# Performance work log

Measured on AMD Instinct MI355X. Metric: run time of the kernel, lower is better.

The kernel has to match this reference:

```python
import jax, jax.numpy as jnp
import numpy as np

B, T, HW = 16, 64, 7
D = 768          # input_dim == base_dim
N = 12           # num_heads
C = D // N       # head_dim = 64
EPS = 1e-5


def layernorm(x, g, b):
    m = jnp.mean(x, axis=-1, keepdims=True)
    v = jnp.mean((x - m) ** 2, axis=-1, keepdims=True)
    return (x - m) * jax.lax.rsqrt(v + EPS) * g + b


def setup_inputs() -> dict:
    key = jax.random.key(0)
    ks = jax.random.split(key, 12)
    s = lambda k, shape: (jax.random.normal(k, shape, jnp.float32) * 0.02)
    return {
        "x": jax.random.normal(ks[0], (B, T, HW, HW, D), jnp.float32),
        "W_qkv": s(ks[1], (D, 3 * D)),                  # qkv_bias=False
        "Wpq": s(ks[2], (C, C, HW, HW)), "bpq": jnp.zeros((C,), jnp.float32),
        "Wpk": s(ks[3], (C, C, HW, HW)), "bpk": jnp.zeros((C,), jnp.float32),
        "Wpv": s(ks[4], (C, C, HW, HW)), "bpv": jnp.zeros((C,), jnp.float32),
        "g_q": jnp.ones((C,), jnp.float32), "be_q": jnp.zeros((C,), jnp.float32),
        "g_k": jnp.ones((C,), jnp.float32), "be_k": jnp.zeros((C,), jnp.float32),
        "g_v": jnp.ones((C,), jnp.float32), "be_v": jnp.zeros((C,), jnp.float32),
        "rel_pos_t": s(ks[5], (2 * T - 1, C)),          # (127, 64): matches dt, no interp
        "W_proj": s(ks[6], (D, D)), "b_proj": jnp.zeros((D,), jnp.float32),
    }


def reference(x, W_qkv, Wpq, bpq, Wpk, bpk, Wpv, bpv,
              g_q, be_q, g_k, be_k, g_v, be_v, rel_pos_t, W_proj, b_proj):
    b, t = x.shape[0], x.shape[1]
    # qkv projection -> (B,T,H,W,3,N,C)
    qkv = (x @ W_qkv).reshape(b, t, HW, HW, 3, N, C)
    q3, k3, v3 = qkv[..., 0, :, :], qkv[..., 1, :, :], qkv[..., 2, :, :]  # (B,T,H,W,N,C)
    # Conv3d kernel (1,7,7) on full 7x7 spatial == contraction over (h,w,c_in)
    q = jnp.einsum('bthwnc,dchw->bntd', q3, Wpq) + bpq   # (B,N,T,C)
    k = jnp.einsum('bthwnc,dchw->bntd', k3, Wpk) + bpk
    v = jnp.einsum('bthwnc,dchw->bntd', v3, Wpv) + bpv
    q = layernorm(q, g_q, be_q)
    k = layernorm(k, g_k, be_k)
    v = layernorm(v, g_v, be_v)
    scale = C ** -0.5
    attn = jnp.einsum('bntc,bnsc->bnts', q * scale, k)   # (B,N,T,T)
    # relative temporal position bias: gather table rows by distance, matmul with q
    dist = jnp.arange(t)[:, None] - jnp.arange(t)[None, :] + (t - 1)  # (T,T) in [0,2T-2]
    Rt = rel_pos_t[dist]                                  # (T,T,C)
    rel = jnp.einsum('bntc,tsc->bnts', q, Rt)
    attn = jax.nn.softmax(attn + rel, axis=-1)
    out = jnp.einsum('bnts,bnsc->bntc', attn, v) + q      # residual add of q
    out = out.transpose(0, 2, 1, 3).reshape(b, t, N * C)  # (B,T,D)
    return out @ W_proj + b_proj
```

## Files before the change

### kernel.cpp

```cpp
#include <hip/hip_runtime.h>


typedef __attribute__((ext_vector_type(8))) short bf16x8;
typedef __attribute__((ext_vector_type(4))) float f32x4;

#define AS1U(p) ((const __attribute__((address_space(1))) unsigned int*)(p))
#define AS3U(p) ((__attribute__((address_space(3))) unsigned int*)(p))

__device__ __forceinline__ unsigned short cvt_bf16(float x) {
  union { float f; unsigned int u; } v; v.f = x;
  unsigned int r = v.u + 0x7fffu + ((v.u >> 16) & 1u);
  return (unsigned short)(r >> 16);
}
__device__ __forceinline__ float bf2f(unsigned short h) {
  union { unsigned int u; float f; } v; v.u = ((unsigned int)h) << 16;
  return v.f;
}

__device__ __forceinline__ void wg_barrier() {
  asm volatile("" ::: "memory");
  __builtin_amdgcn_s_barrier();
  asm volatile("" ::: "memory");
}

__global__ __launch_bounds__(256) void cvt_x_k(const float* __restrict__ src,
                                               unsigned short* __restrict__ dst, int n8) {
  int i = blockIdx.x * 256 + threadIdx.x;
  if (i >= n8) return;
  const float4* s = (const float4*)src + (size_t)i * 2;
  float4 a = s[0], b = s[1];
  ushort4 r0 = { cvt_bf16(a.x), cvt_bf16(a.y), cvt_bf16(a.z), cvt_bf16(a.w) };
  ushort4 r1 = { cvt_bf16(b.x), cvt_bf16(b.y), cvt_bf16(b.z), cvt_bf16(b.w) };
  ushort4* d = (ushort4*)dst + (size_t)i * 2;
  d[0] = r0; d[1] = r1;
}

__global__ __launch_bounds__(256) void transpose_cvt_k(const float* __restrict__ src,
                                                       unsigned short* __restrict__ dst) {
  __shared__ float tl[32][33];
  int k0 = blockIdx.x * 32, n0 = blockIdx.y * 32;
  int tx = threadIdx.x & 31, ty = threadIdx.x >> 5;
#pragma unroll
  for (int r = 0; r < 32; r += 8)
    tl[ty + r][tx] = src[(size_t)(k0 + ty + r) * 2304 + n0 + tx];
  __syncthreads();
#pragma unroll
  for (int r = 0; r < 32; r += 8)
    dst[(size_t)(n0 + ty + r) * 768 + k0 + tx] = cvt_bf16(tl[tx][ty + r]);
}

__global__ __launch_bounds__(256) void prep_cvt_k(
    const float* __restrict__ Wpq, const float* __restrict__ Wpk,
    const float* __restrict__ Wpv, const float* __restrict__ relp,
    unsigned short* __restrict__ WpTT, unsigned short* __restrict__ relb) {
  int bid = blockIdx.x;
  if (bid < 2400) {
    int p = bid / 800;
    const float* src = (p == 0) ? Wpq : (p == 1) ? Wpk : Wpv;
    unsigned short* dst = WpTT + (size_t)p * 204800;
    int o = (bid - p * 800) * 256 + threadIdx.x;
    if (o >= 204800) return;
    int c = o & 63, d = (o >> 6) & 63, hw = o >> 12;
    dst[o] = (hw < 49) ? cvt_bf16(src[d * 3136 + c * 49 + hw]) : (unsigned short)0;
  } else {
    int i = (bid - 2400) * 256 + threadIdx.x;
    relb[i] = (i < 8128) ? cvt_bf16(relp[i]) : (unsigned short)0;
  }
}

__global__ __launch_bounds__(512, 2) void gemm_qkv_8ph(
    const unsigned short* __restrict__ A, const unsigned short* __restrict__ Bt,
    unsigned short* __restrict__ Cb) {
  __shared__ unsigned short As[2][16384];
  __shared__ unsigned short Bs[2][16384];

  const int orig = blockIdx.x;
  const int xcd = orig & 7;
  const int lid = orig >> 3;
  const int wgid = (xcd < 4 ? xcd * 221 : 884 + (xcd - 4) * 220) + lid;
  const int mb = wgid / 9, nb = wgid % 9;
  const int m0 = mb * 256, n0 = nb * 256;
  const int K = 768;

  const int tid = threadIdx.x;
  const int wave = tid >> 6, lane = tid & 63;
  const int quad = lane >> 4, l16 = lane & 15;
  const int wr = wave >> 2, wc = wave & 3;
  const int x7 = l16 & 7;

  const int srow = tid >> 3;
  const int cs = (tid & 7) ^ (srow & 7);
  const unsigned short* Ag[4];
  const unsigned short* Bg[4];
#pragma unroll
  for (int l = 0; l < 4; ++l) {
    Ag[l] = A + (size_t)(m0 + l * 64 + srow) * K + cs * 8;
    Bg[l] = Bt + (size_t)(n0 + l * 64 + srow) * K + cs * 8;
  }
  const int ldst = wave * 512;

#define STAGE(buf, kt) do {                                                        \
    const int ko_ = (kt) * 64;                                                     \
    _Pragma("unroll")                                                              \
    for (int l_ = 0; l_ < 4; ++l_) {                                               \
      __builtin_amdgcn_global_load_lds(AS1U(Ag[l_] + ko_),                         \
          AS3U(&As[buf][l_ * 4096 + ldst]), 16, 0, 0);                             \
      __builtin_amdgcn_global_load_lds(AS1U(Bg[l_] + ko_),                         \
          AS3U(&Bs[buf][l_ * 4096 + ldst]), 16, 0, 0);                             \
    }                                                                              \
  } while (0)

#define LDA(buf, mi) do {                                                          \
    _Pragma("unroll")                                                              \
    for (int fi_ = 0; fi_ < 4; ++fi_) {                                            \
      const int row_ = wr * 128 + (mi) * 64 + fi_ * 16 + l16;                      \
      _Pragma("unroll")                                                            \
      for (int ks_ = 0; ks_ < 2; ++ks_)                                            \
        af[fi_][ks_] = *(const bf16x8*)&As[buf][row_ * 64 +                        \
            (((ks_ * 4 + quad) ^ x7) * 8)];                                        \
    }                                                                              \
  } while (0)

#define LDB(buf, nj) do {                                                          \
    _Pragma("unroll")                                                              \
    for (int fj_ = 0; fj_ < 2; ++fj_) {                                            \
      const int row_ = wc * 64 + (nj) * 32 + fj_ * 16 + l16;                       \
      _Pragma("unroll")                                                            \
      for (int ks_ = 0; ks_ < 2; ++ks_)                                            \
        bfv[nj][fj_][ks_] = *(const bf16x8*)&Bs[buf][row_ * 64 +                   \
            (((ks_ * 4 + quad) ^ x7) * 8)];                                        \
    }                                                                              \
  } while (0)

#define MFMAQ(mi, nj) do {                                                         \
    _Pragma("unroll")                                                              \
    for (int ks_ = 0; ks_ < 2; ++ks_)                                              \
      _Pragma("unroll")                                                            \
      for (int fi_ = 0; fi_ < 4; ++fi_)                                            \
        _Pragma("unroll")                                                          \
        for (int fj_ = 0; fj_ < 2; ++fj_)                                          \
          acc[(mi) * 4 + fi_][(nj) * 2 + fj_] =                                    \
              __builtin_amdgcn_mfma_f32_16x16x32_bf16(af[fi_][ks_],                \
                  bfv[nj][fj_][ks_], acc[(mi) * 4 + fi_][(nj) * 2 + fj_], 0, 0, 0);\
  } while (0)

#define ITER(cur, DO_STAGE, kt2, VMI) do {                                         \
    asm volatile("s_waitcnt vmcnt(" #VMI ")" ::: "memory");                        \
    wg_barrier();                                                                  \
                                                                           \
    LDA(cur, 0); LDB(cur, 0);                                                      \
    wg_barrier();                                                                  \
    __builtin_amdgcn_s_setprio(1); MFMAQ(0, 0); __builtin_amdgcn_s_setprio(0);     \
    wg_barrier();                                                                  \
                                                                           \
    LDB(cur, 1);                                                                   \
    wg_barrier();                                                                  \
    __builtin_amdgcn_s_setprio(1); MFMAQ(0, 1); __builtin_amdgcn_s_setprio(0);     \
    wg_barrier();                                                                  \
                                                                           \
    LDA(cur, 1);                                                                   \
    wg_barrier();                                                                  \
    __builtin_amdgcn_s_setprio(1); MFMAQ(1, 0); __builtin_amdgcn_s_setprio(0);     \
    wg_barrier();                                                                  \
             \
    if (DO_STAGE) STAGE(cur, kt2);                                                 \
    __builtin_amdgcn_s_setprio(1); MFMAQ(1, 1); __builtin_amdgcn_s_setprio(0);     \
    wg_barrier();                                                                  \
  } while (0)

  f32x4 acc[8][4];
#pragma unroll
  for (int i = 0; i < 8; ++i)
#pragma unroll
    for (int j = 0; j < 4; ++j) acc[i][j] = (f32x4){0.f, 0.f, 0.f, 0.f};
  bf16x8 af[4][2];
  bf16x8 bfv[2][2][2];

  STAGE(0, 0);
  STAGE(1, 1);

  for (int kt = 0; kt < 10; kt += 2) {
    ITER(0, true, kt + 2, 8);
    ITER(1, true, kt + 3, 8);
  }
  ITER(0, false, 0, 8);
  ITER(1, false, 0, 0);

#undef ITER
#undef MFMAQ
#undef LDB
#undef LDA
#undef STAGE

#pragma unroll
  for (int i = 0; i < 8; ++i)
#pragma unroll
    for (int j = 0; j < 4; ++j)
#pragma unroll
      for (int r = 0; r < 4; ++r) {
        int row = m0 + wr * 128 + i * 16 + quad * 4 + r;
        int col = n0 + wc * 64 + j * 16 + l16;
        Cb[(size_t)row * 2304 + col] = cvt_bf16(acc[i][j][r]);
      }
}

__global__ __launch_bounds__(256) void pool_ln_mfma_k(
    const unsigned short* __restrict__ qkvb, const unsigned short* __restrict__ WpTT,
    const float* __restrict__ bq, const float* __restrict__ bk, const float* __restrict__ bv,
    const float* __restrict__ gq, const float* __restrict__ gk, const float* __restrict__ gv,
    const float* __restrict__ beq, const float* __restrict__ bek, const float* __restrict__ bev,
    unsigned short* __restrict__ oq, unsigned short* __restrict__ ok_,
    unsigned short* __restrict__ ov) {
  __shared__ float smem_f[16384];
  __shared__ float mu_s[64], rs_s[64];
  unsigned short* AB = (unsigned short*)smem_f;
  float* Ln = smem_f;

  const int n = blockIdx.x, p = blockIdx.y, b = blockIdx.z;
  const int tid = threadIdx.x;
  const int wave = tid >> 6, lane = tid & 63;
  const int quad = lane >> 4, l16 = lane & 15;
  const int wm = (wave >> 1) * 32, wn = (wave & 1) * 32;

  const int lr = lane >> 4, lg = lane & 15;
  const size_t abase = ((size_t)b * 3136) * 2304 + (size_t)p * 768 + (size_t)n * 64;
  const unsigned short* WpB = WpTT + (size_t)p * 204800;

  const unsigned short* pA[4];
  const unsigned short* pB[4];
#pragma unroll
  for (int q = 0; q < 4; ++q) {
    int r = wave * 16 + q * 4 + lr;
    int g = lg ^ (r & 15);
    pA[q] = qkvb + abase + (size_t)r * 112896 + (size_t)(g >> 3) * 2304 + (g & 7) * 8;
    pB[q] = WpB + (size_t)(g >> 3) * 4096 + r * 64 + (g & 7) * 8;
  }

#define PSTAGE(buf, it) do {                                                       \
    const size_t offA_ = (size_t)(it) * 4608;                                      \
    const size_t offB_ = (size_t)(it) * 8192;                                      \
    unsigned short* Ad_ = AB + (buf) * 8192;                                       \
    unsigned short* Bd_ = AB + 16384 + (buf) * 8192;                               \
    _Pragma("unroll")                                                              \
    for (int q_ = 0; q_ < 4; ++q_) {                                               \
      __builtin_amdgcn_global_load_lds(AS1U(pA[q_] + offA_),                       \
          AS3U(&Ad_[(wave * 16 + q_ * 4) * 128]), 16, 0, 0);                       \
      __builtin_amdgcn_global_load_lds(AS1U(pB[q_] + offB_),                       \
          AS3U(&Bd_[(wave * 16 + q_ * 4) * 128]), 16, 0, 0);                       \
    }                                                                              \
  } while (0)

#define PCOMPUTE(buf) do {                                                         \
    const unsigned short* Ad_ = AB + (buf) * 8192;                                 \
    const unsigned short* Bd_ = AB + 16384 + (buf) * 8192;                         \
    bf16x8 af_[2][4], bf_[2][4];                                                   \
    _Pragma("unroll")                                                              \
    for (int f_ = 0; f_ < 2; ++f_) {                                               \
      int ra_ = wm + f_ * 16 + l16;                                                \
      int rb_ = wn + f_ * 16 + l16;                                                \
      _Pragma("unroll")                                                            \
      for (int ki_ = 0; ki_ < 4; ++ki_) {                                          \
        af_[f_][ki_] = *(const bf16x8*)&Ad_[ra_ * 128 +                            \
            (((ki_ * 4 + quad) ^ (ra_ & 15)) * 8)];                                \
        bf_[f_][ki_] = *(const bf16x8*)&Bd_[rb_ * 128 +                            \
            (((ki_ * 4 + quad) ^ (rb_ & 15)) * 8)];                                \
      }                                                                            \
    }                                                                              \
    _Pragma("unroll")                                                              \
    for (int ki_ = 0; ki_ < 4; ++ki_)                                              \
      _Pragma("unroll")                                                            \
      for (int i_ = 0; i_ < 2; ++i_)                                               \
        _Pragma("unroll")                                                          \
        for (int j_ = 0; j_ < 2; ++j_)                                             \
          acc[i_][j_] = __builtin_amdgcn_mfma_f32_16x16x32_bf16(                   \
              af_[i_][ki_], bf_[j_][ki_], acc[i_][j_], 0, 0, 0);                   \
  } while (0)

  f32x4 acc[2][2];
#pragma unroll
  for (int i = 0; i < 2; ++i)
#pragma unroll
    for (int j = 0; j < 2; ++j) acc[i][j] = (f32x4){0.f, 0.f, 0.f, 0.f};

  PSTAGE(0, 0);
  for (int it2 = 0; it2 < 24; it2 += 2) {
    PSTAGE(1, it2 + 1);
    asm volatile("s_waitcnt vmcnt(8)" ::: "memory");
    wg_barrier();
    PCOMPUTE(0);
    wg_barrier();
    PSTAGE(0, it2 + 2);
    asm volatile("s_waitcnt vmcnt(8)" ::: "memory");
    wg_barrier();
    PCOMPUTE(1);
    wg_barrier();
  }
  asm volatile("s_waitcnt vmcnt(0)" ::: "memory");
  wg_barrier();
  PCOMPUTE(0);
  __syncthreads();

#undef PCOMPUTE
#undef PSTAGE

  const float* bias = (p == 0) ? bq : (p == 1) ? bk : bv;
  const float* g    = (p == 0) ? gq : (p == 1) ? gk : gv;
  const float* be   = (p == 0) ? beq : (p == 1) ? bek : bev;
  unsigned short* outp = (p == 0) ? oq : (p == 1) ? ok_ : ov;

#pragma unroll
  for (int i = 0; i < 2; ++i)
#pragma unroll
    for (int j = 0; j < 2; ++j)
#pragma unroll
      for (int r = 0; r < 4; ++r) {
        int t = wm + i * 16 + quad * 4 + r;
        int d = wn + j * 16 + l16;
        Ln[t * 65 + d] = acc[i][j][r] + bias[d];
      }
  __syncthreads();
  if (tid < 64) {
    float s = 0.f;
#pragma unroll 8
    for (int c = 0; c < 64; ++c) s += Ln[tid * 65 + c];
    float m = s * (1.f / 64.f);
    float v2 = 0.f;
#pragma unroll 8
    for (int c = 0; c < 64; ++c) { float dl = Ln[tid * 65 + c] - m; v2 += dl * dl; }
    mu_s[tid] = m;
    rs_s[tid] = rsqrtf(v2 * (1.f / 64.f) + 1e-5f);
  }
  __syncthreads();
  {
    int t = tid >> 2, d0 = (tid & 3) * 16;
    float m = mu_s[t], rv = rs_s[t];
    unsigned short ob[16];
#pragma unroll
    for (int j = 0; j < 16; ++j)
      ob[j] = cvt_bf16((Ln[t * 65 + d0 + j] - m) * rv * g[d0 + j] + be[d0 + j]);
    unsigned short* dst = outp + ((size_t)(b * 12 + n) * 64 + t) * 64 + d0;
    *(uint4*)dst = *(uint4*)ob;
    *(uint4*)(dst + 8) = *(uint4*)(ob + 8);
  }
}

__global__ __launch_bounds__(256) void attn_mfma_k(
    const unsigned short* __restrict__ qp, const unsigned short* __restrict__ kp,
    const unsigned short* __restrict__ vp, const unsigned short* __restrict__ relb,
    float* __restrict__ aout) {
  __shared__ unsigned short qs[64 * 64];
  __shared__ unsigned short ks[64 * 64];
  __shared__ unsigned short vt[64 * 64];
  __shared__ unsigned short rs[128 * 64];
  __shared__ float Gs[64 * 128];
  __shared__ unsigned short Ps[64 * 64];

  const int n = blockIdx.x, b = blockIdx.y;
  const int tid = threadIdx.x;
  const size_t base = ((size_t)b * 12 + n) * 4096;

  for (int i = tid; i < 512; i += 256) {
    ((uint4*)qs)[i] = ((const uint4*)(qp + base))[i];
    ((uint4*)ks)[i] = ((const uint4*)(kp + base))[i];
  }
  for (int i = tid; i < 1024; i += 256)
    ((uint4*)rs)[i] = ((const uint4*)relb)[i];
  {
    int s = tid >> 2, c0 = (tid & 3) * 16;
    unsigned short tmp[16];
    *(uint4*)tmp = *(const uint4*)(vp + base + s * 64 + c0);
    *(uint4*)(tmp + 8) = *(const uint4*)(vp + base + s * 64 + c0 + 8);
#pragma unroll
    for (int i = 0; i < 16; ++i) vt[(c0 + i) * 64 + s] = tmp[i];
  }
  __syncthreads();

  const int wave = tid >> 6, lane = tid & 63;
  const int quad = lane >> 4, l16 = lane & 15;
  const int tm = wave * 16;

  bf16x8 aq[2];
  aq[0] = *(const bf16x8*)&qs[(tm + l16) * 64 + quad * 8];
  aq[1] = *(const bf16x8*)&qs[(tm + l16) * 64 + quad * 8 + 32];

  f32x4 accqk[4], accg[8];
#pragma unroll
  for (int j = 0; j < 4; ++j) accqk[j] = (f32x4){0.f, 0.f, 0.f, 0.f};
#pragma unroll
  for (int j = 0; j < 8; ++j) accg[j] = (f32x4){0.f, 0.f, 0.f, 0.f};

#pragma unroll
  for (int ki = 0; ki < 2; ++ki) {
#pragma unroll
    for (int j = 0; j < 4; ++j) {
      bf16x8 bk = *(const bf16x8*)&ks[(j * 16 + l16) * 64 + quad * 8 + ki * 32];
      accqk[j] = __builtin_amdgcn_mfma_f32_16x16x32_bf16(aq[ki], bk, accqk[j], 0, 0, 0);
    }
#pragma unroll
    for (int j = 0; j < 8; ++j) {
      bf16x8 br = *(const bf16x8*)&rs[(j * 16 + l16) * 64 + quad * 8 + ki * 32];
      accg[j] = __builtin_amdgcn_mfma_f32_16x16x32_bf16(aq[ki], br, accg[j], 0, 0, 0);
    }
  }
#pragma unroll
  for (int j = 0; j < 8; ++j)
#pragma unroll
    for (int r = 0; r < 4; ++r)
      Gs[(tm + quad * 4 + r) * 128 + j * 16 + l16] = accg[j][r];
  __syncthreads();

#pragma unroll
  for (int r = 0; r < 4; ++r) {
    int t = tm + quad * 4 + r;
    float sv[4];
#pragma unroll
    for (int j = 0; j < 4; ++j) {
      int s = j * 16 + l16;
      sv[j] = 0.125f * accqk[j][r] + Gs[t * 128 + (t + 63 - s)];
    }
    float m = fmaxf(fmaxf(sv[0], sv[1]), fmaxf(sv[2], sv[3]));
    m = fmaxf(m, __shfl_xor(m, 1));
    m = fmaxf(m, __shfl_xor(m, 2));
    m = fmaxf(m, __shfl_xor(m, 4));
    m = fmaxf(m, __shfl_xor(m, 8));
    float e[4], sum = 0.f;
#pragma unroll
    for (int j = 0; j < 4; ++j) { e[j] = __expf(sv[j] - m); sum += e[j]; }
    sum += __shfl_xor(sum, 1);
    sum += __shfl_xor(sum, 2);
    sum += __shfl_xor(sum, 4);
    sum += __shfl_xor(sum, 8);
    float inv = 1.f / sum;
#pragma unroll
    for (int j = 0; j < 4; ++j)
      Ps[t * 64 + j * 16 + l16] = cvt_bf16(e[j] * inv);
  }
  __syncthreads();

  bf16x8 ap[2];
  ap[0] = *(const bf16x8*)&Ps[(tm + l16) * 64 + quad * 8];
  ap[1] = *(const bf16x8*)&Ps[(tm + l16) * 64 + quad * 8 + 32];
  f32x4 acco[4];
#pragma unroll
  for (int j = 0; j < 4; ++j) acco[j] = (f32x4){0.f, 0.f, 0.f, 0.f};
#pragma unroll
  for (int ki = 0; ki < 2; ++ki)
#pragma unroll
    for (int j = 0; j < 4; ++j) {
      bf16x8 bv = *(const bf16x8*)&vt[(j * 16 + l16) * 64 + quad * 8 + ki * 32];
      acco[j] = __builtin_amdgcn_mfma_f32_16x16x32_bf16(ap[ki], bv, acco[j], 0, 0, 0);
    }
#pragma unroll
  for (int j = 0; j < 4; ++j)
#pragma unroll
    for (int r = 0; r < 4; ++r) {
      int t = tm + quad * 4 + r;
      int c = j * 16 + l16;
      float o = acco[j][r] + bf2f(qs[t * 64 + c]);
      aout[((size_t)b * 64 + t) * 768 + n * 64 + c] = o;
    }
}

__global__ __launch_bounds__(256) void gemm_f32_k(
    const float* __restrict__ A, const float* __restrict__ Bm,
    const float* __restrict__ bias, float* __restrict__ Cm,
    int M, int Nn, int K) {
  __shared__ float As[16][68];
  __shared__ float Bs[16][64];
  const int tid = threadIdx.x;
  const int ty = tid >> 4, tx = tid & 15;
  const int m0 = blockIdx.y * 64, n0 = blockIdx.x * 64;

  const int la_m = tid >> 2;
  const int la_k = (tid & 3) << 2;
  const int lb_k = tid >> 4;
  const int lb_n = (tid & 15) << 2;

  const float* Ap = A + (size_t)(m0 + la_m) * K + la_k;
  const float* Bp = Bm + (size_t)lb_k * Nn + n0 + lb_n;

  float acc[4][4];
#pragma unroll
  for (int i = 0; i < 4; ++i)
#pragma unroll
    for (int j = 0; j < 4; ++j) acc[i][j] = 0.f;

  for (int k0 = 0; k0 < K; k0 += 16) {
    float4 av = *(const float4*)(Ap + k0);
    float4 bv = *(const float4*)(Bp + (size_t)k0 * Nn);
    As[la_k + 0][la_m] = av.x;
    As[la_k + 1][la_m] = av.y;
    As[la_k + 2][la_m] = av.z;
    As[la_k + 3][la_m] = av.w;
    *(float4*)&Bs[lb_k][lb_n] = bv;
    __syncthreads();
#pragma unroll
    for (int kk = 0; kk < 16; ++kk) {
      float af[4], bf[4];
      *(float4*)af = *(const float4*)&As[kk][ty << 2];
      *(float4*)bf = *(const float4*)&Bs[kk][tx << 2];
#pragma unroll
      for (int i = 0; i < 4; ++i)
#pragma unroll
        for (int j = 0; j < 4; ++j) acc[i][j] += af[i] * bf[j];
    }
    __syncthreads();
  }

  float bb[4] = {0.f, 0.f, 0.f, 0.f};
  if (bias) {
#pragma unroll
    for (int j = 0; j < 4; ++j) bb[j] = bias[n0 + (tx << 2) + j];
  }
#pragma unroll
  for (int i = 0; i < 4; ++i) {
    float4 o;
    o.x = acc[i][0] + bb[0];
    o.y = acc[i][1] + bb[1];
    o.z = acc[i][2] + bb[2];
    o.w = acc[i][3] + bb[3];
    *(float4*)(Cm + (size_t)(m0 + (ty << 2) + i) * Nn + n0 + (tx << 2)) = o;
  }
}

extern "C" void kernel_launch(void* const* d_in, const int* in_sizes, int n_in,
                              void* d_out, int out_size, void* d_ws, size_t ws_size,
                              hipStream_t stream) {
  const float* x     = (const float*)d_in[0];
  const float* Wqkv  = (const float*)d_in[1];
  const float* Wpq   = (const float*)d_in[2];
  const float* bpq   = (const float*)d_in[3];
  const float* Wpk   = (const float*)d_in[4];
  const float* bpk   = (const float*)d_in[5];
  const float* Wpv   = (const float*)d_in[6];
  const float* bpv   = (const float*)d_in[7];
  const float* gq    = (const float*)d_in[8];
  const float* beq   = (const float*)d_in[9];
  const float* gk    = (const float*)d_in[10];
  const float* bek   = (const float*)d_in[11];
  const float* gv    = (const float*)d_in[12];
  const float* bev   = (const float*)d_in[13];
  const float* relp  = (const float*)d_in[14];
  const float* Wproj = (const float*)d_in[15];
  const float* bproj = (const float*)d_in[16];
  float* out = (float*)d_out;

  unsigned short* u = (unsigned short*)d_ws;
  unsigned short* xbf   = u;
  unsigned short* qkvbf = u + 38535168ull;
  unsigned short* WqkvT = u + 154140672ull;
  unsigned short* WpTT  = u + 155910144ull;
  unsigned short* relb  = u + 156524544ull;
  unsigned short* qpb   = u + 156532736ull;
  unsigned short* kpb   = u + 157319168ull;
  unsigned short* vpb   = u + 158105600ull;
  float* aout = (float*)(u + 158892032ull);

  cvt_x_k<<<18816, 256, 0, stream>>>(x, xbf, 4816896);
  transpose_cvt_k<<<dim3(24, 72), 256, 0, stream>>>(Wqkv, WqkvT);
  prep_cvt_k<<<2432, 256, 0, stream>>>(Wpq, Wpk, Wpv, relp, WpTT, relb);

  gemm_qkv_8ph<<<1764, 512, 0, stream>>>(xbf, WqkvT, qkvbf);

  pool_ln_mfma_k<<<dim3(12, 3, 16), 256, 0, stream>>>(
      qkvbf, WpTT, bpq, bpk, bpv, gq, gk, gv, beq, bek, bev, qpb, kpb, vpb);

  attn_mfma_k<<<dim3(12, 16), 256, 0, stream>>>(qpb, kpb, vpb, relb, aout);

  gemm_f32_k<<<dim3(12, 16), 256, 0, stream>>>(aout, Wproj, bproj, out, 1024, 768, 768);
}
```

Baseline: 617.2 us.

## Shrink QKV GEMM tile to 128x128 with 256 threads and XCD-aware mapping

Replaces the 256x256, 512-thread QKV projection GEMM with a 128x128 tile on 256 threads, launching four times as many workgroups. Tiles are now assigned so each XCD owns a contiguous band of row blocks across all column blocks. Staging is split into separate A and B loads placed at different points in the four-phase MFMA schedule, and fragments are held in separate register arrays for the two halves. The smaller tile cuts LDS and registers per workgroup, allowing more occupancy and better load balance. The cost is lower arithmetic intensity per tile and more global and L2 traffic.

```diff
diff --git a/kernel.cpp b/kernel.cpp
--- a/kernel.cpp
+++ b/kernel.cpp
@@ -68,24 +68,24 @@
   }
 }
 
-__global__ __launch_bounds__(512, 2) void gemm_qkv_8ph(
+__global__ __launch_bounds__(256, 2) void gemm_qkv_128(
     const unsigned short* __restrict__ A, const unsigned short* __restrict__ Bt,
     unsigned short* __restrict__ Cb) {
-  __shared__ unsigned short As[2][16384];
-  __shared__ unsigned short Bs[2][16384];
+  __shared__ unsigned short As[2][8192];
+  __shared__ unsigned short Bs[2][8192];
 
   const int orig = blockIdx.x;
   const int xcd = orig & 7;
-  const int lid = orig >> 3;
-  const int wgid = (xcd < 4 ? xcd * 221 : 884 + (xcd - 4) * 220) + lid;
-  const int mb = wgid / 9, nb = wgid % 9;
-  const int m0 = mb * 256, n0 = nb * 256;
+  const int slot = orig >> 3;
+  const int mb = xcd * 49 + slot / 18;
+  const int nb = slot % 18;
+  const int m0 = mb * 128, n0 = nb * 128;
   const int K = 768;
 
   const int tid = threadIdx.x;
   const int wave = tid >> 6, lane = tid & 63;
   const int quad = lane >> 4, l16 = lane & 15;
-  const int wr = wave >> 2, wc = wave & 3;
+  const int wr = wave >> 1, wc = wave & 1;
   const int x7 = l16 & 7;
 
   const int srow = tid >> 3;
@@ -94,90 +94,99 @@
   const unsigned short* Bg[4];
 #pragma unroll
   for (int l = 0; l < 4; ++l) {
-    Ag[l] = A + (size_t)(m0 + l * 64 + srow) * K + cs * 8;
-    Bg[l] = Bt + (size_t)(n0 + l * 64 + srow) * K + cs * 8;
+    Ag[l] = A + (size_t)(m0 + l * 32 + srow) * K + cs * 8;
+    Bg[l] = Bt + (size_t)(n0 + l * 32 + srow) * K + cs * 8;
   }
   const int ldst = wave * 512;
 
-#define STAGE(buf, kt) do {                                                        \
+#define STAGE_A(buf, kt) do {                                                      \
     const int ko_ = (kt) * 64;                                                     \
     _Pragma("unroll")                                                              \
-    for (int l_ = 0; l_ < 4; ++l_) {                                               \
+    for (int l_ = 0; l_ < 4; ++l_)                                                 \
       __builtin_amdgcn_global_load_lds(AS1U(Ag[l_] + ko_),                         \
-          AS3U(&As[buf][l_ * 4096 + ldst]), 16, 0, 0);                             \
+          AS3U(&As[buf][l_ * 2048 + ldst]), 16, 0, 0);                             \
+  } while (0)
+
+#define STAGE_B(buf, kt) do {                                                      \
+    const int ko_ = (kt) * 64;                                                     \
+    _Pragma("unroll")                                                              \
+    for (int l_ = 0; l_ < 4; ++l_)                                                 \
       __builtin_amdgcn_global_load_lds(AS1U(Bg[l_] + ko_),                         \
-          AS3U(&Bs[buf][l_ * 4096 + ldst]), 16, 0, 0);                             \
-    }                                                                              \
-  } while (0)
-
-#define LDA(buf, mi) do {                                                          \
-    _Pragma("unroll")                                                              \
-    for (int fi_ = 0; fi_ < 4; ++fi_) {                                            \
-      const int row_ = wr * 128 + (mi) * 64 + fi_ * 16 + l16;                      \
+          AS3U(&Bs[buf][l_ * 2048 + ldst]), 16, 0, 0);                             \
+  } while (0)
+
+#define LDA(dst, buf, mi) do {                                                     \
+    _Pragma("unroll")                                                              \
+    for (int fi_ = 0; fi_ < 2; ++fi_) {                                            \
+      const int row_ = wr * 64 + (mi) * 32 + fi_ * 16 + l16;                       \
       _Pragma("unroll")                                                            \
       for (int ks_ = 0; ks_ < 2; ++ks_)                                            \
-        af[fi_][ks_] = *(const bf16x8*)&As[buf][row_ * 64 +                        \
+        dst[fi_][ks_] = *(const bf16x8*)&As[buf][row_ * 64 +                       \
             (((ks_ * 4 + quad) ^ x7) * 8)];                                        \
     }                                                                              \
   } while (0)
 
-#define LDB(buf, nj) do {                                                          \
+#define LDB(dst, buf, nj) do {                                                     \
     _Pragma("unroll")                                                              \
     for (int fj_ = 0; fj_ < 2; ++fj_) {                                            \
       const int row_ = wc * 64 + (nj) * 32 + fj_ * 16 + l16;                       \
       _Pragma("unroll")                                                            \
       for (int ks_ = 0; ks_ < 2; ++ks_)                                            \
-        bfv[nj][fj_][ks_] = *(const bf16x8*)&Bs[buf][row_ * 64 +                   \
+        dst[fj_][ks_] = *(const bf16x8*)&Bs[buf][row_ * 64 +                       \
             (((ks_ * 4 + quad) ^ x7) * 8)];                                        \
     }                                                                              \
   } while (0)
 
-#define MFMAQ(mi, nj) do {                                                         \
+#define MFMAQ(a_, b_, mi, nj) do {                                                 \
     _Pragma("unroll")                                                              \
     for (int ks_ = 0; ks_ < 2; ++ks_)                                              \
       _Pragma("unroll")                                                            \
-      for (int fi_ = 0; fi_ < 4; ++fi_)                                            \
+      for (int fi_ = 0; fi_ < 2; ++fi_)                                            \
         _Pragma("unroll")                                                          \
         for (int fj_ = 0; fj_ < 2; ++fj_)                                          \
-          acc[(mi) * 4 + fi_][(nj) * 2 + fj_] =                                    \
-              __builtin_amdgcn_mfma_f32_16x16x32_bf16(af[fi_][ks_],                \
-                  bfv[nj][fj_][ks_], acc[(mi) * 4 + fi_][(nj) * 2 + fj_], 0, 0, 0);\
+          acc[(mi) * 2 + fi_][(nj) * 2 + fj_] =                                    \
+              __builtin_amdgcn_mfma_f32_16x16x32_bf16(a_[fi_][ks_],                \
+                  b_[fj_][ks_], acc[(mi) * 2 + fi_][(nj) * 2 + fj_], 0, 0, 0);     \
   } while (0)
 
 #define ITER(cur, DO_STAGE, kt2, VMI) do {                                         \
     asm volatile("s_waitcnt vmcnt(" #VMI ")" ::: "memory");                        \
     wg_barrier();                                                                  \
-                                                                           \
-    LDA(cur, 0); LDB(cur, 0);                                                      \
-    wg_barrier();                                                                  \
-    __builtin_amdgcn_s_setprio(1); MFMAQ(0, 0); __builtin_amdgcn_s_setprio(0);     \
-    wg_barrier();                                                                  \
-                                                                           \
-    LDB(cur, 1);                                                                   \
-    wg_barrier();                                                                  \
-    __builtin_amdgcn_s_setprio(1); MFMAQ(0, 1); __builtin_amdgcn_s_setprio(0);     \
-    wg_barrier();                                                                  \
-                                                                           \
-    LDA(cur, 1);                                                                   \
-    wg_barrier();                                                                  \
-    __builtin_amdgcn_s_setprio(1); MFMAQ(1, 0); __builtin_amdgcn_s_setprio(0);     \
-    wg_barrier();                                                                  \
-             \
-    if (DO_STAGE) STAGE(cur, kt2);                                                 \
-    __builtin_amdgcn_s_setprio(1); MFMAQ(1, 1); __builtin_amdgcn_s_setprio(0);     \
-    wg_barrier();                                                                  \
-  } while (0)
-
-  f32x4 acc[8][4];
-#pragma unroll
-  for (int i = 0; i < 8; ++i)
+                                                           \
+    LDA(af0, cur, 0); LDB(bf0, cur, 0);                                            \
+    wg_barrier();                                                                  \
+    __builtin_amdgcn_s_setprio(1); MFMAQ(af0, bf0, 0, 0);                          \
+    __builtin_amdgcn_s_setprio(0);                                                 \
+    wg_barrier();                                                                  \
+                                                           \
+    LDB(bf1, cur, 1);                                                              \
+    wg_barrier();                                                                  \
+    __builtin_amdgcn_s_setprio(1); MFMAQ(af0, bf1, 0, 1);                          \
+    __builtin_amdgcn_s_setprio(0);                                                 \
+    wg_barrier();                                                                  \
+           \
+    LDA(af1, cur, 1);                                                              \
+    if (DO_STAGE) STAGE_B(cur, kt2);                                               \
+    wg_barrier();                                                                  \
+    __builtin_amdgcn_s_setprio(1); MFMAQ(af1, bf0, 1, 0);                          \
+    __builtin_amdgcn_s_setprio(0);                                                 \
+    wg_barrier();                                                                  \
+           \
+    if (DO_STAGE) STAGE_A(cur, kt2);                                               \
+    __builtin_amdgcn_s_setprio(1); MFMAQ(af1, bf1, 1, 1);                          \
+    __builtin_amdgcn_s_setprio(0);                                                 \
+    wg_barrier();                                                                  \
+  } while (0)
+
+  f32x4 acc[4][4];
+#pragma unroll
+  for (int i = 0; i < 4; ++i)
 #pragma unroll
     for (int j = 0; j < 4; ++j) acc[i][j] = (f32x4){0.f, 0.f, 0.f, 0.f};
-  bf16x8 af[4][2];
-  bf16x8 bfv[2][2][2];
-
-  STAGE(0, 0);
-  STAGE(1, 1);
+  bf16x8 af0[2][2], af1[2][2], bf0[2][2], bf1[2][2];
+
+  STAGE_B(0, 0); STAGE_A(0, 0);
+  STAGE_B(1, 1); STAGE_A(1, 1);
 
   for (int kt = 0; kt < 10; kt += 2) {
     ITER(0, true, kt + 2, 8);
@@ -190,15 +199,16 @@
 #undef MFMAQ
 #undef LDB
 #undef LDA
-#undef STAGE
-
-#pragma unroll
-  for (int i = 0; i < 8; ++i)
+#undef STAGE_B
+#undef STAGE_A
+
+#pragma unroll
+  for (int i = 0; i < 4; ++i)
 #pragma unroll
     for (int j = 0; j < 4; ++j)
 #pragma unroll
       for (int r = 0; r < 4; ++r) {
-        int row = m0 + wr * 128 + i * 16 + quad * 4 + r;
+        int row = m0 + wr * 64 + i * 16 + quad * 4 + r;
         int col = n0 + wc * 64 + j * 16 + l16;
         Cb[(size_t)row * 2304 + col] = cvt_bf16(acc[i][j][r]);
       }
@@ -560,7 +570,7 @@
   transpose_cvt_k<<<dim3(24, 72), 256, 0, stream>>>(Wqkv, WqkvT);
   prep_cvt_k<<<2432, 256, 0, stream>>>(Wpq, Wpk, Wpv, relp, WpTT, relb);
 
-  gemm_qkv_8ph<<<1764, 512, 0, stream>>>(xbf, WqkvT, qkvbf);
+  gemm_qkv_128<<<7056, 256, 0, stream>>>(xbf, WqkvT, qkvbf);
 
   pool_ln_mfma_k<<<dim3(12, 3, 16), 256, 0, stream>>>(
       qkvbf, WpTT, bpq, bpk, bpv, gq, gk, gv, beq, bek, bev, qpb, kpb, vpb);
```

Result: faster. 604.2 us (-2.1%).
